# Kernel optimization log

Measured on AMD Instinct MI355X. Metric: run time of the kernel, lower is better.

The kernel has to match this reference:

```python
import jax, jax.numpy as jnp
import numpy as np

VOCAB = 256
UNITS = 512

def setup_inputs() -> dict:
    key = jax.random.key(0)
    ks = jax.random.split(key, 7)
    B, T = 64, 1024
    scale = 0.02
    return {
        "inputs": jax.random.randint(ks[0], (B, T), 0, VOCAB, dtype=jnp.int32),
        "emb": jax.random.normal(ks[1], (VOCAB, VOCAB), dtype=jnp.float32) * scale,
        "Wx": jax.random.normal(ks[2], (VOCAB, UNITS), dtype=jnp.float32) * scale,
        "Wh": jax.random.normal(ks[3], (UNITS, UNITS), dtype=jnp.float32) * scale,
        "b": jnp.zeros((UNITS,), dtype=jnp.float32),
        "Wd": jax.random.normal(ks[4], (UNITS, VOCAB), dtype=jnp.float32) * scale,
        "bd": jnp.zeros((VOCAB,), dtype=jnp.float32),
    }

def reference(inputs, emb, Wx, Wh, b, Wd, bd):
    # Embedding lookup: [B, T] -> [B, T, VOCAB]
    x = emb[inputs]
    B = x.shape[0]
    # Precompute input projection for all timesteps (one big GEMM)
    xp = jnp.einsum("bte,eu->btu", x, Wx) + b  # [B, T, U]
    h0 = jnp.zeros((B, Wh.shape[0]), dtype=x.dtype)

    def step(h, xp_t):
        h_new = jnp.tanh(xp_t + h @ Wh)  # SimpleRNN cell: tanh(x W_x + h W_h + b)
        return h_new, h_new

    _, hs = jax.lax.scan(step, h0, jnp.swapaxes(xp, 0, 1))  # hs: [T, B, U]
    hs = jnp.swapaxes(hs, 0, 1)  # [B, T, U]
    logits = jnp.einsum("btu,uv->btv", hs, Wd) + bd  # [B, T, VOCAB]
    return logits
```

## Files before the change

### kernel.cpp

```cpp
#include <hip/hip_runtime.h>
#include <math.h>

#define BB   64
#define TT_  1024
#define UU   512
#define VV   256
#define EE   256
#define TC   64
#define NUG  8
#define NBG  32

__device__ __forceinline__ float tanh_fast(float x) {
    float e = __expf(x + x);
    return 1.f - 2.f * __builtin_amdgcn_rcpf(e + 1.f);
}

__global__ __launch_bounds__(512) void e2_kernel(
    const float* __restrict__ emb, const float* __restrict__ Wx,
    const float* __restrict__ bias, float* __restrict__ E2)
{
    const int v = blockIdx.x;
    const int u = threadIdx.x;
    float acc = bias[u];
    const float* er = emb + v * EE;
    #pragma unroll 8
    for (int e = 0; e < EE; ++e)
        acc = fmaf(er[e], Wx[e * UU + u], acc);
    E2[v * UU + u] = acc;
}

__global__ __launch_bounds__(512, 2) void rnn_chunk_kernel(
    const int* __restrict__ toks, const float* __restrict__ E2,
    const float* __restrict__ Wh, unsigned long long* hpub,
    float* __restrict__ hs, int t0)
{
    __shared__ float WhLDS[UU * 64];
    __shared__ float hstage[8][2][64];
    __shared__ float partials[2][8][2][64];
    __shared__ int   stok[2][TC];

    const int bid  = blockIdx.x;
    const int ug   = bid & 7;
    const int bg   = bid >> 3;
    const int tid  = threadIdx.x;
    const int w    = tid >> 6;
    const int lane = tid & 63;
    const int u4   = lane & 15;
    const int kq   = lane >> 4;
    const int b0   = bg * 2;

    const float4* Wh4  = (const float4*)Wh;
    float4*       WhL4 = (float4*)WhLDS;
    {
        const int col = tid & 15;
        const int kr0 = tid >> 4;
        #pragma unroll
        for (int p = 0; p < 16; ++p) {
            int k = p * 32 + kr0;
            WhL4[k * 16 + col] = Wh4[k * 128 + ug * 16 + col];
        }
    }
    if (tid < 128) {
        int b = tid >> 6, q = tid & 63;
        stok[b][q] = toks[(b0 + b) * TT_ + t0 + q];
    }
    __syncthreads();

    for (int tt = 0; tt < TC; ++tt) {
        const int s = t0 + tt;

        float xp = 0.f;
        if (w < 2) xp = E2[stok[w][tt] * UU + ug * 64 + lane];

        float hreg[2][16];
        if (s > 0) {
            const int slot = (s - 1) & 1;
            unsigned long long* src0 = hpub + ((size_t)slot * BB + b0)     * UU + w * 64 + lane;
            unsigned long long* src1 = hpub + ((size_t)slot * BB + b0 + 1) * UU + w * 64 + lane;
            unsigned long long p0 = __hip_atomic_load(src0, __ATOMIC_RELAXED, __HIP_MEMORY_SCOPE_AGENT);
            unsigned long long p1 = __hip_atomic_load(src1, __ATOMIC_RELAXED, __HIP_MEMORY_SCOPE_AGENT);
            const unsigned int want = (unsigned int)(s - 1);
            while (true) {
                unsigned long long ok0 = __ballot((unsigned int)(p0 >> 32) == want);
                unsigned long long ok1 = __ballot((unsigned int)(p1 >> 32) == want);
                if ((ok0 & ok1) == 0xFFFFFFFFFFFFFFFFull) break;
                __builtin_amdgcn_s_sleep(1);
                p0 = __hip_atomic_load(src0, __ATOMIC_RELAXED, __HIP_MEMORY_SCOPE_AGENT);
                p1 = __hip_atomic_load(src1, __ATOMIC_RELAXED, __HIP_MEMORY_SCOPE_AGENT);
            }
            hstage[w][0][lane] = __uint_as_float((unsigned int)p0);
            hstage[w][1][lane] = __uint_as_float((unsigned int)p1);
            const float4* h40 = (const float4*)hstage[w][0];
            const float4* h41 = (const float4*)hstage[w][1];
            #pragma unroll
            for (int r = 0; r < 4; ++r) {
                float4 a = h40[kq * 4 + r];
                hreg[0][4*r+0] = a.x; hreg[0][4*r+1] = a.y;
                hreg[0][4*r+2] = a.z; hreg[0][4*r+3] = a.w;
                float4 c = h41[kq * 4 + r];
                hreg[1][4*r+0] = c.x; hreg[1][4*r+1] = c.y;
                hreg[1][4*r+2] = c.z; hreg[1][4*r+3] = c.w;
            }
        }

        float acc0[4] = {0.f,0.f,0.f,0.f};
        float acc1[4] = {0.f,0.f,0.f,0.f};
        if (s > 0) {
            #pragma unroll
            for (int j = 0; j < 16; ++j) {
                float4 wv = WhL4[(w * 64 + kq * 16 + j) * 16 + u4];
                float ha = hreg[0][j], hb = hreg[1][j];
                acc0[0] = fmaf(ha, wv.x, acc0[0]);
                acc0[1] = fmaf(ha, wv.y, acc0[1]);
                acc0[2] = fmaf(ha, wv.z, acc0[2]);
                acc0[3] = fmaf(ha, wv.w, acc0[3]);
                acc1[0] = fmaf(hb, wv.x, acc1[0]);
                acc1[1] = fmaf(hb, wv.y, acc1[1]);
                acc1[2] = fmaf(hb, wv.z, acc1[2]);
                acc1[3] = fmaf(hb, wv.w, acc1[3]);
            }
        }

        #pragma unroll
        for (int i = 0; i < 4; ++i) {
            acc0[i] += __shfl_xor(acc0[i], 16, 64);
            acc0[i] += __shfl_xor(acc0[i], 32, 64);
            acc1[i] += __shfl_xor(acc1[i], 16, 64);
            acc1[i] += __shfl_xor(acc1[i], 32, 64);
        }
        if (kq == 0) {
            *(float4*)&partials[s & 1][w][0][u4 * 4] =
                make_float4(acc0[0], acc0[1], acc0[2], acc0[3]);
            *(float4*)&partials[s & 1][w][1][u4 * 4] =
                make_float4(acc1[0], acc1[1], acc1[2], acc1[3]);
        }
        __syncthreads();

        if (w < 2) {
            float ssum = xp;
            #pragma unroll
            for (int wv = 0; wv < 8; ++wv)
                ssum += partials[s & 1][wv][w][lane];
            float h = tanh_fast(ssum);
            hs[((size_t)(b0 + w) * TC + tt) * UU + ug * 64 + lane] = h;
            unsigned long long pk =
                ((unsigned long long)(unsigned int)s << 32) | __float_as_uint(h);
            __hip_atomic_store(hpub + ((size_t)(s & 1) * BB + (b0 + w)) * UU + ug * 64 + lane,
                               pk, __ATOMIC_RELAXED, __HIP_MEMORY_SCOPE_AGENT);
        }
    }
}

#define GM 64
#define GN 64
#define GK 16

__global__ __launch_bounds__(256) void logits_kernel(
    const float* __restrict__ A,
    const float* __restrict__ Wd,
    const float* __restrict__ bd,
    float* __restrict__ out, int t0)
{
    __shared__ float As[GK][GM + 1];
    __shared__ float Bs[GK][GN + 1];
    const int tid  = threadIdx.x;
    const int row0 = blockIdx.x * GM;
    const int col0 = blockIdx.y * GN;
    const int tm = tid >> 4;
    const int tn = tid & 15;

    float acc[4][4] = {{0.f}};

    for (int k0 = 0; k0 < UU; k0 += GK) {
        #pragma unroll
        for (int i = 0; i < 4; ++i) {
            int lidx = i * 256 + tid;
            int r = lidx >> 4;
            int c = lidx & 15;
            As[c][r] = A[(row0 + r) * UU + k0 + c];
        }
        #pragma unroll
        for (int i = 0; i < 4; ++i) {
            int lidx = i * 256 + tid;
            int c = lidx >> 6;
            int n = lidx & 63;
            Bs[c][n] = Wd[(k0 + c) * VV + col0 + n];
        }
        __syncthreads();
        #pragma unroll
        for (int kk = 0; kk < GK; ++kk) {
            float av[4], bv[4];
            #pragma unroll
            for (int i = 0; i < 4; ++i) av[i] = As[kk][tm * 4 + i];
            #pragma unroll
            for (int j = 0; j < 4; ++j) bv[j] = Bs[kk][tn * 4 + j];
            #pragma unroll
            for (int i = 0; i < 4; ++i)
                #pragma unroll
                for (int j = 0; j < 4; ++j)
                    acc[i][j] = fmaf(av[i], bv[j], acc[i][j]);
        }
        __syncthreads();
    }

    #pragma unroll
    for (int i = 0; i < 4; ++i) {
        int r  = row0 + tm * 4 + i;
        int bb = r / TC;
        int tt = r & (TC - 1);
        float4 res;
        res.x = acc[i][0] + bd[col0 + tn * 4 + 0];
        res.y = acc[i][1] + bd[col0 + tn * 4 + 1];
        res.z = acc[i][2] + bd[col0 + tn * 4 + 2];
        res.w = acc[i][3] + bd[col0 + tn * 4 + 3];
        *(float4*)(out + (size_t)(bb * TT_ + t0 + tt) * VV + col0 + tn * 4) = res;
    }
}

extern "C" void kernel_launch(void* const* d_in, const int* in_sizes, int n_in,
                              void* d_out, int out_size, void* d_ws, size_t ws_size,
                              hipStream_t stream)
{
    (void)in_sizes; (void)n_in; (void)out_size; (void)ws_size;

    const int*   toks = (const int*)  d_in[0];
    const float* emb  = (const float*)d_in[1];
    const float* Wx   = (const float*)d_in[2];
    const float* Wh   = (const float*)d_in[3];
    const float* bias = (const float*)d_in[4];
    const float* Wd   = (const float*)d_in[5];
    const float* bd   = (const float*)d_in[6];
    float* out = (float*)d_out;

    unsigned long long* hpub = (unsigned long long*)d_ws;
    float* E2 = (float*)(hpub + 2 * BB * UU);
    float* hs = E2 + EE * UU;

    e2_kernel<<<EE, UU, 0, stream>>>(emb, Wx, bias, E2);

    for (int c = 0; c < TT_ / TC; ++c) {
        const int t0 = c * TC;
        rnn_chunk_kernel<<<NBG * NUG, 512, 0, stream>>>(toks, E2, Wh, hpub, hs, t0);
        logits_kernel<<<dim3((BB * TC) / GM, VV / GN), 256, 0, stream>>>(hs, Wd, bd, out, t0);
    }
}
```

Before: 2.775 ms.

## Fuse output projection into recurrent kernel via atomic accumulation, add volatile spin fast path

```diff
diff --git a/kernel.cpp b/kernel.cpp
--- a/kernel.cpp
+++ b/kernel.cpp
@@ -7,8 +7,6 @@
 #define VV   256
 #define EE   256
 #define TC   64
-#define NUG  8
-#define NBG  32
 
 __device__ __forceinline__ float tanh_fast(float x) {
     float e = __expf(x + x);
@@ -31,17 +29,20 @@
 
 __global__ __launch_bounds__(512, 2) void rnn_chunk_kernel(
     const int* __restrict__ toks, const float* __restrict__ E2,
-    const float* __restrict__ Wh, unsigned long long* hpub,
-    float* __restrict__ hs, int t0)
+    const float* __restrict__ Wh, const float* __restrict__ Wd,
+    const float* __restrict__ bd,
+    unsigned long long* hpub,
+    float* out, int t0, int last)
 {
     __shared__ float WhLDS[UU * 64];
     __shared__ float hstage[8][2][64];
     __shared__ float partials[2][8][2][64];
+    __shared__ float hmine[2][2][64];
     __shared__ int   stok[2][TC];
 
     const int bid  = blockIdx.x;
-    const int ug   = bid & 7;
-    const int bg   = bid >> 3;
+    const int bg   = bid & 31;
+    const int ug   = bid >> 5;
     const int tid  = threadIdx.x;
     const int w    = tid >> 6;
     const int lane = tid & 63;
@@ -64,29 +65,60 @@
         int b = tid >> 6, q = tid & 63;
         stok[b][q] = toks[(b0 + b) * TT_ + t0 + q];
     }
+    if (t0 > 0 && tid < 128) {
+        int b = tid >> 6, u = tid & 63;
+        unsigned long long p =
+            hpub[((size_t)((t0 - 1) & 1) * BB + (b0 + b)) * UU + ug * 64 + u];
+        hmine[(t0 - 1) & 1][b][u] = __uint_as_float((unsigned int)p);
+    }
+
+    const int bmine = w & 1;
+    const int vmine = (w >> 1) * 64 + lane;
+    float wdreg[64];
+    #pragma unroll
+    for (int u = 0; u < 64; ++u)
+        wdreg[u] = Wd[(ug * 64 + u) * VV + vmine];
+    const float bdv = (ug == 0) ? bd[vmine] : 0.f;
+
     __syncthreads();
 
+    int fails = 0;
     for (int tt = 0; tt < TC; ++tt) {
         const int s = t0 + tt;
-
         float xp = 0.f;
         if (w < 2) xp = E2[stok[w][tt] * UU + ug * 64 + lane];
 
-        float hreg[2][16];
+        float acc0[4] = {0.f,0.f,0.f,0.f};
+        float acc1[4] = {0.f,0.f,0.f,0.f};
         if (s > 0) {
             const int slot = (s - 1) & 1;
-            unsigned long long* src0 = hpub + ((size_t)slot * BB + b0)     * UU + w * 64 + lane;
-            unsigned long long* src1 = hpub + ((size_t)slot * BB + b0 + 1) * UU + w * 64 + lane;
-            unsigned long long p0 = __hip_atomic_load(src0, __ATOMIC_RELAXED, __HIP_MEMORY_SCOPE_AGENT);
-            unsigned long long p1 = __hip_atomic_load(src1, __ATOMIC_RELAXED, __HIP_MEMORY_SCOPE_AGENT);
             const unsigned int want = (unsigned int)(s - 1);
-            while (true) {
-                unsigned long long ok0 = __ballot((unsigned int)(p0 >> 32) == want);
-                unsigned long long ok1 = __ballot((unsigned int)(p1 >> 32) == want);
-                if ((ok0 & ok1) == 0xFFFFFFFFFFFFFFFFull) break;
-                __builtin_amdgcn_s_sleep(1);
-                p0 = __hip_atomic_load(src0, __ATOMIC_RELAXED, __HIP_MEMORY_SCOPE_AGENT);
-                p1 = __hip_atomic_load(src1, __ATOMIC_RELAXED, __HIP_MEMORY_SCOPE_AGENT);
+            unsigned long long* a0 = hpub + ((size_t)slot * BB + b0) * UU + w * 64 + lane;
+            unsigned long long* a1 = a0 + UU;
+            unsigned long long p0 = 0, p1 = 0;
+            bool got = false;
+            if (fails < 3) {
+                volatile const unsigned long long* f0 = a0;
+                volatile const unsigned long long* f1 = a1;
+                for (int it = 0; it < 24; ++it) {
+                    p0 = *f0; p1 = *f1;
+                    unsigned long long ok =
+                        __ballot((unsigned int)(p0 >> 32) == want) &
+                        __ballot((unsigned int)(p1 >> 32) == want);
+                    if (ok == 0xFFFFFFFFFFFFFFFFull) { got = true; break; }
+                }
+                if (!got) ++fails;
+            }
+            if (!got) {
+                while (true) {
+                    p0 = __hip_atomic_load(a0, __ATOMIC_RELAXED, __HIP_MEMORY_SCOPE_AGENT);
+                    p1 = __hip_atomic_load(a1, __ATOMIC_RELAXED, __HIP_MEMORY_SCOPE_AGENT);
+                    unsigned long long ok =
+                        __ballot((unsigned int)(p0 >> 32) == want) &
+                        __ballot((unsigned int)(p1 >> 32) == want);
+                    if (ok == 0xFFFFFFFFFFFFFFFFull) break;
+                    __builtin_amdgcn_s_sleep(1);
+                }
             }
             hstage[w][0][lane] = __uint_as_float((unsigned int)p0);
             hstage[w][1][lane] = __uint_as_float((unsigned int)p1);
@@ -95,29 +127,21 @@
             #pragma unroll
             for (int r = 0; r < 4; ++r) {
                 float4 a = h40[kq * 4 + r];
-                hreg[0][4*r+0] = a.x; hreg[0][4*r+1] = a.y;
-                hreg[0][4*r+2] = a.z; hreg[0][4*r+3] = a.w;
                 float4 c = h41[kq * 4 + r];
-                hreg[1][4*r+0] = c.x; hreg[1][4*r+1] = c.y;
-                hreg[1][4*r+2] = c.z; hreg[1][4*r+3] = c.w;
-            }
-        }
-
-        float acc0[4] = {0.f,0.f,0.f,0.f};
-        float acc1[4] = {0.f,0.f,0.f,0.f};
-        if (s > 0) {
-            #pragma unroll
-            for (int j = 0; j < 16; ++j) {
-                float4 wv = WhL4[(w * 64 + kq * 16 + j) * 16 + u4];
-                float ha = hreg[0][j], hb = hreg[1][j];
-                acc0[0] = fmaf(ha, wv.x, acc0[0]);
-                acc0[1] = fmaf(ha, wv.y, acc0[1]);
-                acc0[2] = fmaf(ha, wv.z, acc0[2]);
-                acc0[3] = fmaf(ha, wv.w, acc0[3]);
-                acc1[0] = fmaf(hb, wv.x, acc1[0]);
-                acc1[1] = fmaf(hb, wv.y, acc1[1]);
-                acc1[2] = fmaf(hb, wv.z, acc1[2]);
-                acc1[3] = fmaf(hb, wv.w, acc1[3]);
+                float ha[4] = {a.x, a.y, a.z, a.w};
+                float hc[4] = {c.x, c.y, c.z, c.w};
+                #pragma unroll
+                for (int q = 0; q < 4; ++q) {
+                    float4 wv = WhL4[(w * 64 + kq * 16 + r * 4 + q) * 16 + u4];
+                    acc0[0] = fmaf(ha[q], wv.x, acc0[0]);
+                    acc0[1] = fmaf(ha[q], wv.y, acc0[1]);
+                    acc0[2] = fmaf(ha[q], wv.z, acc0[2]);
+                    acc0[3] = fmaf(ha[q], wv.w, acc0[3]);
+                    acc1[0] = fmaf(hc[q], wv.x, acc1[0]);
+                    acc1[1] = fmaf(hc[q], wv.y, acc1[1]);
+                    acc1[2] = fmaf(hc[q], wv.z, acc1[2]);
+                    acc1[3] = fmaf(hc[q], wv.w, acc1[3]);
+                }
             }
         }
 
@@ -142,78 +166,44 @@
             for (int wv = 0; wv < 8; ++wv)
                 ssum += partials[s & 1][wv][w][lane];
             float h = tanh_fast(ssum);
-            hs[((size_t)(b0 + w) * TC + tt) * UU + ug * 64 + lane] = h;
             unsigned long long pk =
                 ((unsigned long long)(unsigned int)s << 32) | __float_as_uint(h);
-            __hip_atomic_store(hpub + ((size_t)(s & 1) * BB + (b0 + w)) * UU + ug * 64 + lane,
-                               pk, __ATOMIC_RELAXED, __HIP_MEMORY_SCOPE_AGENT);
-        }
-    }
-}
-
-#define GM 64
-#define GN 64
-#define GK 16
-
-__global__ __launch_bounds__(256) void logits_kernel(
-    const float* __restrict__ A,
-    const float* __restrict__ Wd,
-    const float* __restrict__ bd,
-    float* __restrict__ out, int t0)
-{
-    __shared__ float As[GK][GM + 1];
-    __shared__ float Bs[GK][GN + 1];
-    const int tid  = threadIdx.x;
-    const int row0 = blockIdx.x * GM;
-    const int col0 = blockIdx.y * GN;
-    const int tm = tid >> 4;
-    const int tn = tid & 15;
-
-    float acc[4][4] = {{0.f}};
-
-    for (int k0 = 0; k0 < UU; k0 += GK) {
+            unsigned long long* dst =
+                hpub + ((size_t)(s & 1) * BB + (b0 + w)) * UU + ug * 64 + lane;
+            *(volatile unsigned long long*)dst = pk;
+            __hip_atomic_store(dst, pk, __ATOMIC_RELAXED, __HIP_MEMORY_SCOPE_AGENT);
+            hmine[s & 1][w][lane] = h;
+        }
+
+        if (s > 0) {
+            const float4* hb = (const float4*)hmine[(s - 1) & 1][bmine];
+            float sum = bdv;
+            #pragma unroll
+            for (int j = 0; j < 16; ++j) {
+                float4 h4 = hb[j];
+                sum = fmaf(h4.x, wdreg[4*j+0], sum);
+                sum = fmaf(h4.y, wdreg[4*j+1], sum);
+                sum = fmaf(h4.z, wdreg[4*j+2], sum);
+                sum = fmaf(h4.w, wdreg[4*j+3], sum);
+            }
+            atomicAdd(out + ((size_t)(b0 + bmine) * TT_ + (s - 1)) * VV + vmine, sum);
+        }
+    }
+
+    if (last) {
+        __syncthreads();
+        const int s = t0 + TC - 1;
+        const float4* hb = (const float4*)hmine[s & 1][bmine];
+        float sum = bdv;
         #pragma unroll
-        for (int i = 0; i < 4; ++i) {
-            int lidx = i * 256 + tid;
-            int r = lidx >> 4;
-            int c = lidx & 15;
-            As[c][r] = A[(row0 + r) * UU + k0 + c];
-        }
-        #pragma unroll
-        for (int i = 0; i < 4; ++i) {
-            int lidx = i * 256 + tid;
-            int c = lidx >> 6;
-            int n = lidx & 63;
-            Bs[c][n] = Wd[(k0 + c) * VV + col0 + n];
-        }
-        __syncthreads();
-        #pragma unroll
-        for (int kk = 0; kk < GK; ++kk) {
-            float av[4], bv[4];
-            #pragma unroll
-            for (int i = 0; i < 4; ++i) av[i] = As[kk][tm * 4 + i];
-            #pragma unroll
-            for (int j = 0; j < 4; ++j) bv[j] = Bs[kk][tn * 4 + j];
-            #pragma unroll
-            for (int i = 0; i < 4; ++i)
-                #pragma unroll
-                for (int j = 0; j < 4; ++j)
-                    acc[i][j] = fmaf(av[i], bv[j], acc[i][j]);
-        }
-        __syncthreads();
-    }
-
-    #pragma unroll
-    for (int i = 0; i < 4; ++i) {
-        int r  = row0 + tm * 4 + i;
-        int bb = r / TC;
-        int tt = r & (TC - 1);
-        float4 res;
-        res.x = acc[i][0] + bd[col0 + tn * 4 + 0];
-        res.y = acc[i][1] + bd[col0 + tn * 4 + 1];
-        res.z = acc[i][2] + bd[col0 + tn * 4 + 2];
-        res.w = acc[i][3] + bd[col0 + tn * 4 + 3];
-        *(float4*)(out + (size_t)(bb * TT_ + t0 + tt) * VV + col0 + tn * 4) = res;
+        for (int j = 0; j < 16; ++j) {
+            float4 h4 = hb[j];
+            sum = fmaf(h4.x, wdreg[4*j+0], sum);
+            sum = fmaf(h4.y, wdreg[4*j+1], sum);
+            sum = fmaf(h4.z, wdreg[4*j+2], sum);
+            sum = fmaf(h4.w, wdreg[4*j+3], sum);
+        }
+        atomicAdd(out + ((size_t)(b0 + bmine) * TT_ + s) * VV + vmine, sum);
     }
 }
 
@@ -221,7 +211,7 @@
                               void* d_out, int out_size, void* d_ws, size_t ws_size,
                               hipStream_t stream)
 {
-    (void)in_sizes; (void)n_in; (void)out_size; (void)ws_size;
+    (void)in_sizes; (void)n_in; (void)ws_size;
 
     const int*   toks = (const int*)  d_in[0];
     const float* emb  = (const float*)d_in[1];
@@ -234,13 +224,13 @@
 
     unsigned long long* hpub = (unsigned long long*)d_ws;
     float* E2 = (float*)(hpub + 2 * BB * UU);
-    float* hs = E2 + EE * UU;
-
+
+    hipMemsetAsync(out, 0, (size_t)out_size * sizeof(float), stream);
     e2_kernel<<<EE, UU, 0, stream>>>(emb, Wx, bias, E2);
 
     for (int c = 0; c < TT_ / TC; ++c) {
         const int t0 = c * TC;
-        rnn_chunk_kernel<<<NBG * NUG, 512, 0, stream>>>(toks, E2, Wh, hpub, hs, t0);
-        logits_kernel<<<dim3((BB * TC) / GM, VV / GN), 256, 0, stream>>>(hs, Wd, bd, out, t0);
-    }
-}
+        rnn_chunk_kernel<<<256, 512, 0, stream>>>(
+            toks, E2, Wh, Wd, bd, hpub, out, t0, c == (TT_ / TC - 1));
+    }
+}
```

Result: faster. 2.664 ms (-4.0%).
